# Performance work log

Measured on AMD Instinct MI355X. Metric: run time of the kernel, lower is better.

## Reference

```python
import jax, jax.numpy as jnp
import numpy as np

HID = 2048
NEXP = 16
BRD = max(64, HID // 8)        # block_router_dim = 256
BATCH, SEQ = 4, 8192
BASE_BS, MAX_BS = 512, 2048
BASE_THR, BASE_BUDGET = 0.6, 0.3


def _adjust(seq_len):
    # mirrors _adjust_parameters_for_length (static: depends only on shape)
    if seq_len <= 4096:
        return BASE_BS, BASE_THR, BASE_BUDGET
    elif seq_len <= 16384:
        return min(1024, MAX_BS), BASE_THR * 1.1, BASE_BUDGET * 0.7
    else:
        scale = min(seq_len / 16384, 4)
        return min(int(BASE_BS * scale), MAX_BS), BASE_THR * 1.2, BASE_BUDGET * (1.0 / scale)


def _layernorm(x, g, b, eps=1e-5):
    m = x.mean(-1, keepdims=True)
    v = ((x - m) ** 2).mean(-1, keepdims=True)
    return (x - m) / jnp.sqrt(v + eps) * g + b


def setup_inputs() -> dict:
    key = jax.random.key(0)
    k = jax.random.split(key, 6)
    return {
        "hidden_states": jax.random.normal(k[0], (BATCH, SEQ, HID), jnp.float32),
        # block_router: Linear(H->256) -> LN -> GELU -> Linear(256->E)
        "bw1": jax.random.normal(k[1], (HID, BRD), jnp.float32) * 0.02,
        "bb1": jnp.zeros((BRD,), jnp.float32),
        "ln_g": jnp.ones((BRD,), jnp.float32),
        "ln_b": jnp.zeros((BRD,), jnp.float32),
        # final block-router layer scaled up so block entropies spread around the
        # 0.66 threshold and both routing branches are exercised
        "bw2": jax.random.normal(k[2], (BRD, NEXP), jnp.float32) * 0.6,
        "bb2": jnp.zeros((NEXP,), jnp.float32),
        # token_router: Linear(H->H/2) -> GELU -> (Dropout: eval/identity) -> Linear(H/2->E)
        "tw1": jax.random.normal(k[3], (HID, HID // 2), jnp.float32) * 0.02,
        "tb1": jnp.zeros((HID // 2,), jnp.float32),
        "tw2": jax.random.normal(k[4], (HID // 2, NEXP), jnp.float32) * 0.02,
        "tb2": jnp.zeros((NEXP,), jnp.float32),
    }


def reference(hidden_states, bw1, bb1, ln_g, ln_b, bw2, bb2, tw1, tb1, tw2, tb2):
    B, S, H = hidden_states.shape
    E = bw2.shape[1]
    bs, thr, budget = _adjust(S)
    assert S % bs == 0, "reference assumes seq_len divisible by block_size"
    N = S // bs
    max_tok = int(S * budget)               # python int (static)
    k_budget = max(1, max_tok // bs)        # blocks_within_budget (static)

    # --- block-level routing ---
    block_repr = hidden_states.reshape(B, N, bs, H).mean(2)          # [B,N,H]
    h = _layernorm(block_repr @ bw1 + bb1, ln_g, ln_b)
    block_logits = jax.nn.gelu(h, approximate=False) @ bw2 + bb2     # [B,N,E]
    block_probs = jax.nn.softmax(block_logits, -1)
    p = block_probs + 1e-10
    entropy = -jnp.sum(p * jnp.log(p), -1) / jnp.log(jnp.float32(E))  # [B,N]

    mask1 = entropy > thr
    total_high = mask1.sum()
    # budget-based threshold adjustment (k-th largest high entropy)
    flat_ent = jnp.where(mask1.ravel(), entropy.ravel(), -jnp.inf)
    kth = jnp.sort(flat_ent)[::-1][k_budget - 1]
    cond = (total_high * bs > max_tok) & (total_high > 0) & (k_budget < total_high)
    mask2 = jnp.where(cond, entropy > kth, mask1)

    # sequential token budget over flattened (batch, block) row-major order
    cum = jnp.cumsum(mask2.ravel().astype(jnp.int32) * bs).reshape(B, N)
    token_flag = mask2 & (cum <= max_tok)            # per-token routing
    block_flag = (~mask1) | (mask2 & ~token_flag)    # block-level routing

    # block weight scatter: argmax one-hot * max prob (detached, torch uses .item())
    bw = jax.lax.stop_gradient(
        jax.nn.one_hot(jnp.argmax(block_probs, -1), E, dtype=block_probs.dtype)
        * jnp.max(block_probs, -1, keepdims=True))   # [B,N,E]

    # token-level routing computed densely, masked (dropout in eval mode = identity)
    th = jax.nn.gelu(hidden_states @ tw1 + tb1, approximate=False)
    token_probs = jax.nn.softmax(th @ tw2 + tb2, -1)  # [B,S,E]

    tf = jnp.repeat(token_flag, bs, axis=1)[..., None]   # [B,S,1]
    bf = jnp.repeat(block_flag, bs, axis=1)[..., None]
    bw_tok = jnp.repeat(bw, bs, axis=1)                  # [B,S,E]
    routing = jnp.where(tf, token_probs, jnp.where(bf, bw_tok, jnp.zeros((), hidden_states.dtype)))

    usage = routing.mean((0, 1))
    target = 1.0 / E
    aux = jnp.sum(target * jnp.log(target / (usage + 1e-10)))
    return routing, aux
```

## Files before the change

kernel.cpp:

```cpp
#include <hip/hip_runtime.h>
#include <math.h>

#define BB 4
#define SS 8192
#define HH 2048
#define EE 16
#define BRD_ 256
#define BSZ 1024
#define NN 8
#define NB 32
#define MAXTOK 1720
#define HHALF 1024
#define TC 16
#define ROWS 64
#define KSP 32
#define KL 64
#define JL 64

typedef __attribute__((ext_vector_type(8))) short bf16x8;
typedef __attribute__((ext_vector_type(4))) float f32x4;

__device__ inline short f2bf(float f) {
  unsigned u = __builtin_bit_cast(unsigned, f);
  u += 0x7FFFu + ((u >> 16) & 1u);
  return (short)(u >> 16);
}

__device__ inline void wave_flags(const double* __restrict__ ent, int l,
                                  int& flag_out, int& fb_out) {
  const double THR = 0.6 * 1.1;
  double e = (l < NB) ? ent[l] : -INFINITY;
  bool m1 = (l < NB) && (e > THR);
  unsigned long long m1mask = __ballot(m1);
  int th = __popcll(m1mask);
  double sel = m1 ? e : -INFINITY;
  #pragma unroll
  for (int o = 32; o; o >>= 1) sel = fmax(sel, __shfl_xor(sel, o));
  bool m2 = (th >= 2) ? ((l < NB) && (e > sel)) : m1;
  unsigned long long m2mask = __ballot(m2);
  int cum = __popcll(m2mask & ((2ULL << l) - 1ULL)) * BSZ;
  bool tf = m2 && (cum <= MAXTOK);
  bool bf = (l < NB) && ((!m1) || (m2 && !tf));
  flag_out = tf ? 1 : (bf ? 2 : 0);
  unsigned long long tfmask = __ballot(tf);
  fb_out = tfmask ? (__ffsll(tfmask) - 1) : -1;
}

__global__ __launch_bounds__(256) void k_bmean(const float* __restrict__ x,
                                               double* __restrict__ part) {
  int wg = blockIdx.x;
  int bn = wg >> 4, tc = wg & 15;
  int b = bn >> 3, n = bn & 7;
  int tid = threadIdx.x;
  const float* base = x + ((size_t)(b * SS + n * BSZ + tc * ROWS) * HH);
  double a0=0,a1=0,a2=0,a3=0,a4=0,a5=0,a6=0,a7=0;
  #pragma unroll 4
  for (int t = 0; t < ROWS; ++t) {
    const float4* r = (const float4*)(base + (size_t)t * HH);
    float4 u = r[tid];
    float4 v = r[tid + 256];
    a0 += u.x; a1 += u.y; a2 += u.z; a3 += u.w;
    a4 += v.x; a5 += v.y; a6 += v.z; a7 += v.w;
  }
  double* p = part + ((size_t)bn * TC + tc) * HH;
  int hA = tid * 4, hB = 1024 + tid * 4;
  p[hA] = a0; p[hA+1] = a1; p[hA+2] = a2; p[hA+3] = a3;
  p[hB] = a4; p[hB+1] = a5; p[hB+2] = a6; p[hB+3] = a7;
}

__global__ __launch_bounds__(256) void k_g1(const double* __restrict__ part,
    const float* __restrict__ bw1, double* __restrict__ g1part) {
  __shared__ double brs[NB][KL];
  __shared__ float  wsm[KL][JL];
  int bid = blockIdx.x;
  int kq = bid >> 2, jt = bid & 3;
  int k0 = kq * KL, j0 = jt * JL;
  int tid = threadIdx.x;
  #pragma unroll
  for (int i = 0; i < 8; ++i) {
    int e = i * 256 + tid;
    int bn = e >> 6, k = e & 63;
    const double* pp = part + ((size_t)bn * TC) * HH + k0 + k;
    double s = 0;
    #pragma unroll
    for (int tc = 0; tc < TC; ++tc) s += pp[(size_t)tc * HH];
    brs[bn][k] = s * (1.0 / BSZ);
  }
  #pragma unroll
  for (int i = 0; i < 4; ++i) {
    int f = i * 256 + tid;
    int r = f >> 4, c4 = f & 15;
    float4 v = *(const float4*)(bw1 + (size_t)(k0 + r) * BRD_ + j0 + c4 * 4);
    *(float4*)&wsm[r][c4 * 4] = v;
  }
  __syncthreads();
  int j = tid & 63;
  int bh = (tid >> 6) * 8;
  double acc[8];
  #pragma unroll
  for (int r = 0; r < 8; ++r) acc[r] = 0;
  #pragma unroll 8
  for (int k = 0; k < KL; ++k) {
    double wv = (double)wsm[k][j];
    #pragma unroll
    for (int r = 0; r < 8; ++r) acc[r] += brs[bh + r][k] * wv;
  }
  #pragma unroll
  for (int r = 0; r < 8; ++r)
    g1part[((size_t)kq * NB + bh + r) * BRD_ + j0 + j] = acc[r];
}

__global__ __launch_bounds__(256) void k_router2(const double* __restrict__ g1part,
    const float* __restrict__ bb1, const float* __restrict__ lng, const float* __restrict__ lnb,
    const float* __restrict__ bw2, const float* __restrict__ bb2,
    double* __restrict__ ent, float* __restrict__ bwv, int* __restrict__ bwi) {
  __shared__ double tg[BRD_];
  __shared__ double p3[16][EE];
  __shared__ double red[4];
  __shared__ double l2[EE];
  __shared__ double bcast;
  int bn = blockIdx.x, tid = threadIdx.x;

  double a = (double)bb1[tid];
  #pragma unroll
  for (int kq = 0; kq < KSP; ++kq) a += g1part[((size_t)kq * NB + bn) * BRD_ + tid];

  double v = a;
  for (int o = 32; o; o >>= 1) v += __shfl_down(v, o);
  if ((tid & 63) == 0) red[tid >> 6] = v;
  __syncthreads();
  if (tid == 0) bcast = (red[0] + red[1] + red[2] + red[3]) * (1.0 / BRD_);
  __syncthreads();
  double m = bcast;
  double d = a - m;
  v = d * d;
  for (int o = 32; o; o >>= 1) v += __shfl_down(v, o);
  if ((tid & 63) == 0) red[tid >> 6] = v;
  __syncthreads();
  if (tid == 0) bcast = (red[0] + red[1] + red[2] + red[3]) * (1.0 / BRD_);
  __syncthreads();
  double var = bcast;
  double xn = d / sqrt(var + 1e-5) * (double)lng[tid] + (double)lnb[tid];
  tg[tid] = 0.5 * xn * (1.0 + erf(xn * 0.7071067811865476));
  __syncthreads();

  {
    int e = tid & 15, jc = tid >> 4;
    double s = 0;
    const float* w2 = bw2 + (size_t)(jc * 16) * EE + e;
    #pragma unroll
    for (int jj = 0; jj < 16; ++jj) s += tg[jc * 16 + jj] * (double)w2[jj * EE];
    p3[jc][e] = s;
  }
  __syncthreads();
  if (tid < EE) {
    double acc = (double)bb2[tid];
    #pragma unroll
    for (int jc = 0; jc < 16; ++jc) acc += p3[jc][tid];
    l2[tid] = acc;
  }
  __syncthreads();

  if (tid < 64) {
    int e = tid & 15;
    double le = l2[e];
    double mx = le;
    #pragma unroll
    for (int o = 1; o < 16; o <<= 1) mx = fmax(mx, __shfl_xor(mx, o));
    double pe = exp(le - mx);
    double se = pe;
    #pragma unroll
    for (int o = 1; o < 16; o <<= 1) se += __shfl_xor(se, o);
    double pr = pe / se;
    double q = pr + 1e-10;
    double term = -q * log(q);
    double es = term;
    #pragma unroll
    for (int o = 1; o < 16; o <<= 1) es += __shfl_xor(es, o);
    double mp = pr;
    #pragma unroll
    for (int o = 1; o < 16; o <<= 1) mp = fmax(mp, __shfl_xor(mp, o));
    unsigned long long eqm = __ballot((tid < 16) && (pr == mp));
    if (tid == 0) {
      ent[bn] = es / log(16.0);
      bwv[bn] = (float)mp;
      bwi[bn] = __ffsll(eqm) - 1;
    }
  }
}

__global__ __launch_bounds__(256) void k_out(const double* __restrict__ ent,
    const float* __restrict__ bwv, const int* __restrict__ bwi,
    const float* __restrict__ x, const float* __restrict__ tw1, const float* __restrict__ tb1,
    const float* __restrict__ tw2, float* __restrict__ routing, float* __restrict__ lpart) {
  __shared__ int flg_s[NB + 1];
  __shared__ short xs_bf[64][72];
  __shared__ short wsT[64][72];
  __shared__ float ths[64][65];
  int tid = threadIdx.x;
  int bid = blockIdx.x;
  if (tid < 64) {
    int f, fb;
    wave_flags(ent, tid, f, fb);
    if (tid < NB) flg_s[tid] = f;
    if (tid == 0) flg_s[NB] = fb;
  }
  __syncthreads();

  if (bid < 256) {
    int bn = bid >> 3, seg = bid & 7;
    int fl = flg_s[bn];
    if (fl == 1) return;
    int b = bn >> 3, n = bn & 7;
    float4 z = make_float4(0.f, 0.f, 0.f, 0.f);
    float4 val = z;
    int c_hit = -1;
    if (fl == 2) {
      int ai = bwi[bn];
      c_hit = ai >> 2;
      ((float*)&val)[ai & 3] = bwv[bn];
    }
    float4* out = (float4*)(routing + ((size_t)(b * SS + n * BSZ + seg * 128) * EE));
    #pragma unroll
    for (int l = 0; l < 2; ++l) {
      int idx = l * 256 + tid;
      int c = idx & 3;
      out[idx] = (c == c_hit) ? val : z;
    }
    return;
  }

  int fb = flg_s[NB];
  if (fb < 0) return;
  int b = fb >> 3, n = fb & 7;
  int tb = bid - 256;
  int tg = tb >> 4, nc = tb & 15;
  int t0 = tg * 64, j0 = nc * 64;
  const float* xb = x + ((size_t)(b * SS + n * BSZ + t0) * HH);
  int wv = tid >> 6, lane = tid & 63;
  int wm = (wv >> 1) * 32, wn = (wv & 1) * 32;
  int fr = lane & 15, kg = lane >> 4;
  f32x4 acc00 = {0,0,0,0}, acc01 = {0,0,0,0}, acc10 = {0,0,0,0}, acc11 = {0,0,0,0};

  for (int k0 = 0; k0 < HH; k0 += 64) {
    #pragma unroll
    for (int i = 0; i < 16; ++i) {
      int e = i * 256 + tid; int r = e >> 6, c = e & 63;
      xs_bf[r][c] = f2bf(xb[(size_t)r * HH + k0 + c]);
    }
    #pragma unroll
    for (int i = 0; i < 16; ++i) {
      int e = i * 256 + tid; int r = e >> 6, c = e & 63;
      wsT[c][r] = f2bf(tw1[(size_t)(k0 + r) * HHALF + j0 + c]);
    }
    __syncthreads();
    #pragma unroll
    for (int kc = 0; kc < 64; kc += 32) {
      int ks = kc + kg * 8;
      bf16x8 a0 = *(const bf16x8*)&xs_bf[wm + fr][ks];
      bf16x8 a1 = *(const bf16x8*)&xs_bf[wm + 16 + fr][ks];
      bf16x8 b0 = *(const bf16x8*)&wsT[wn + fr][ks];
      bf16x8 b1 = *(const bf16x8*)&wsT[wn + 16 + fr][ks];
      acc00 = __builtin_amdgcn_mfma_f32_16x16x32_bf16(a0, b0, acc00, 0, 0, 0);
      acc01 = __builtin_amdgcn_mfma_f32_16x16x32_bf16(a0, b1, acc01, 0, 0, 0);
      acc10 = __builtin_amdgcn_mfma_f32_16x16x32_bf16(a1, b0, acc10, 0, 0, 0);
      acc11 = __builtin_amdgcn_mfma_f32_16x16x32_bf16(a1, b1, acc11, 0, 0, 0);
    }
    __syncthreads();
  }
  #pragma unroll
  for (int r = 0; r < 4; ++r) {
    int row0 = wm + kg * 4 + r, row1 = wm + 16 + kg * 4 + r;
    int col0 = wn + fr,         col1 = wn + 16 + fr;
    float v00 = acc00[r] + tb1[j0 + col0];
    float v01 = acc01[r] + tb1[j0 + col1];
    float v10 = acc10[r] + tb1[j0 + col0];
    float v11 = acc11[r] + tb1[j0 + col1];
    ths[row0][col0] = 0.5f * v00 * (1.0f + erff(v00 * 0.70710678f));
    ths[row0][col1] = 0.5f * v01 * (1.0f + erff(v01 * 0.70710678f));
    ths[row1][col0] = 0.5f * v10 * (1.0f + erff(v10 * 0.70710678f));
    ths[row1][col1] = 0.5f * v11 * (1.0f + erff(v11 * 0.70710678f));
  }
  __syncthreads();
  float* lp = lpart + (size_t)nc * (BSZ * EE);
  #pragma unroll
  for (int l = 0; l < 4; ++l) {
    int idx = l * 256 + tid; int t = idx >> 4, e = idx & 15;
    float s = 0;
    #pragma unroll
    for (int jj = 0; jj < 64; ++jj) s += ths[t][jj] * tw2[(size_t)(j0 + jj) * EE + e];
    lp[(t0 + t) * EE + e] = s;
  }
}

__global__ __launch_bounds__(1024) void k_tail(const double* __restrict__ ent,
    const float* __restrict__ lpart, const float* __restrict__ tb2,
    const float* __restrict__ bwv, const int* __restrict__ bwi,
    float* __restrict__ routing, float* __restrict__ outaux) {
  __shared__ int flg_s[NB + 1];
  __shared__ double up[16][EE];
  __shared__ double us[EE];
  int tid = threadIdx.x;
  if (tid < 64) {
    int f, fb;
    wave_flags(ent, tid, f, fb);
    if (tid < NB) flg_s[tid] = f;
    if (tid == 0) flg_s[NB] = fb;
  }
  __syncthreads();
  int fb = flg_s[NB];
  if (fb >= 0) {
    int b = fb >> 3, n = fb & 7;
    int t = tid;
    float l[EE];
    #pragma unroll
    for (int e = 0; e < EE; ++e) {
      float s = tb2[e];
      #pragma unroll
      for (int nc = 0; nc < 16; ++nc) s += lpart[(size_t)nc * (BSZ * EE) + t * EE + e];
      l[e] = s;
    }
    float mx = l[0];
    for (int e = 1; e < EE; ++e) mx = fmaxf(mx, l[e]);
    float se = 0;
    for (int e = 0; e < EE; ++e) { l[e] = expf(l[e] - mx); se += l[e]; }
    float inv = 1.0f / se;
    for (int e = 0; e < EE; ++e) l[e] *= inv;
    float4* orow = (float4*)(routing + ((size_t)(b * SS + n * BSZ + t) * EE));
    orow[0] = make_float4(l[0], l[1], l[2], l[3]);
    orow[1] = make_float4(l[4], l[5], l[6], l[7]);
    orow[2] = make_float4(l[8], l[9], l[10], l[11]);
    orow[3] = make_float4(l[12], l[13], l[14], l[15]);
    int w = tid >> 6;
    for (int e = 0; e < EE; ++e) {
      double v = (double)l[e];
      for (int o = 32; o; o >>= 1) v += __shfl_down(v, o);
      if ((tid & 63) == 0) up[w][e] = v;
    }
  }
  __syncthreads();
  if (tid < EE) {
    double s = 0;
    if (fb >= 0) for (int w = 0; w < 16; ++w) s += up[w][tid];
    for (int i = 0; i < NB; ++i)
      if (flg_s[i] == 2 && bwi[i] == tid) s += (double)BSZ * (double)bwv[i];
    us[tid] = s;
  }
  __syncthreads();
  if (tid == 0) {
    double aux = 0;
    const double target = 1.0 / EE;
    for (int e = 0; e < EE; ++e) {
      double u = us[e] / (double)(BB * SS);
      aux += target * log(target / (u + 1e-10));
    }
    *outaux = (float)aux;
  }
}

extern "C" void kernel_launch(void* const* d_in, const int* in_sizes, int n_in,
                              void* d_out, int out_size, void* d_ws, size_t ws_size,
                              hipStream_t stream) {
  const float* x   = (const float*)d_in[0];
  const float* bw1 = (const float*)d_in[1];
  const float* bb1 = (const float*)d_in[2];
  const float* lng = (const float*)d_in[3];
  const float* lnb = (const float*)d_in[4];
  const float* bw2 = (const float*)d_in[5];
  const float* bb2 = (const float*)d_in[6];
  const float* tw1 = (const float*)d_in[7];
  const float* tb1 = (const float*)d_in[8];
  const float* tw2 = (const float*)d_in[9];
  const float* tb2 = (const float*)d_in[10];
  float* routing = (float*)d_out;
  float* outaux = routing + (size_t)BB * SS * EE;

  char* w = (char*)d_ws;
  size_t off = 0;
  double* part  = (double*)(w + off); off += (size_t)NB * TC * HH * 8;
  double* g1p   = (double*)(w + off); off += (size_t)KSP * NB * BRD_ * 8;
  float*  lpart = (float*) (w + off); off += 16 * (size_t)BSZ * EE * 4;
  double* ent   = (double*)(w + off); off += NB * 8;
  float*  bwv   = (float*) (w + off); off += 256;
  int*    bwi   = (int*)   (w + off); off += 256;

  hipLaunchKernelGGL(k_bmean,   dim3(NB * TC), dim3(256),  0, stream, x, part);
  hipLaunchKernelGGL(k_g1,      dim3(128),     dim3(256),  0, stream, part, bw1, g1p);
  hipLaunchKernelGGL(k_router2, dim3(NB),      dim3(256),  0, stream, g1p,
                     bb1, lng, lnb, bw2, bb2, ent, bwv, bwi);
  hipLaunchKernelGGL(k_out,     dim3(512),     dim3(256),  0, stream, ent, bwv, bwi,
                     x, tw1, tb1, tw2, routing, lpart);
  hipLaunchKernelGGL(k_tail,    dim3(1),       dim3(1024), 0, stream, ent, lpart, tb2,
                     bwv, bwi, routing, outaux);
}
```

Baseline: 75.12 us.

## Fuse five kernels into two using last-block-done atomic counters

```diff
diff --git a/kernel.cpp b/kernel.cpp
--- a/kernel.cpp
+++ b/kernel.cpp
@@ -11,11 +11,8 @@
 #define NB 32
 #define MAXTOK 1720
 #define HHALF 1024
-#define TC 16
-#define ROWS 64
-#define KSP 32
-#define KL 64
-#define JL 64
+#define TC 32
+#define ROWS 32
 
 typedef __attribute__((ext_vector_type(8))) short bf16x8;
 typedef __attribute__((ext_vector_type(4))) float f32x4;
@@ -46,84 +43,79 @@
   fb_out = tfmask ? (__ffsll(tfmask) - 1) : -1;
 }
 
-__global__ __launch_bounds__(256) void k_bmean(const float* __restrict__ x,
-                                               double* __restrict__ part) {
-  int wg = blockIdx.x;
-  int bn = wg >> 4, tc = wg & 15;
-  int b = bn >> 3, n = bn & 7;
-  int tid = threadIdx.x;
-  const float* base = x + ((size_t)(b * SS + n * BSZ + tc * ROWS) * HH);
-  double a0=0,a1=0,a2=0,a3=0,a4=0,a5=0,a6=0,a7=0;
-  #pragma unroll 4
-  for (int t = 0; t < ROWS; ++t) {
-    const float4* r = (const float4*)(base + (size_t)t * HH);
-    float4 u = r[tid];
-    float4 v = r[tid + 256];
-    a0 += u.x; a1 += u.y; a2 += u.z; a3 += u.w;
-    a4 += v.x; a5 += v.y; a6 += v.z; a7 += v.w;
-  }
-  double* p = part + ((size_t)bn * TC + tc) * HH;
-  int hA = tid * 4, hB = 1024 + tid * 4;
-  p[hA] = a0; p[hA+1] = a1; p[hA+2] = a2; p[hA+3] = a3;
-  p[hB] = a4; p[hB+1] = a5; p[hB+2] = a6; p[hB+3] = a7;
-}
-
-__global__ __launch_bounds__(256) void k_g1(const double* __restrict__ part,
-    const float* __restrict__ bw1, double* __restrict__ g1part) {
-  __shared__ double brs[NB][KL];
-  __shared__ float  wsm[KL][JL];
-  int bid = blockIdx.x;
-  int kq = bid >> 2, jt = bid & 3;
-  int k0 = kq * KL, j0 = jt * JL;
-  int tid = threadIdx.x;
-  #pragma unroll
-  for (int i = 0; i < 8; ++i) {
-    int e = i * 256 + tid;
-    int bn = e >> 6, k = e & 63;
-    const double* pp = part + ((size_t)bn * TC) * HH + k0 + k;
-    double s = 0;
-    #pragma unroll
-    for (int tc = 0; tc < TC; ++tc) s += pp[(size_t)tc * HH];
-    brs[bn][k] = s * (1.0 / BSZ);
-  }
-  #pragma unroll
-  for (int i = 0; i < 4; ++i) {
-    int f = i * 256 + tid;
-    int r = f >> 4, c4 = f & 15;
-    float4 v = *(const float4*)(bw1 + (size_t)(k0 + r) * BRD_ + j0 + c4 * 4);
-    *(float4*)&wsm[r][c4 * 4] = v;
-  }
-  __syncthreads();
-  int j = tid & 63;
-  int bh = (tid >> 6) * 8;
-  double acc[8];
-  #pragma unroll
-  for (int r = 0; r < 8; ++r) acc[r] = 0;
-  #pragma unroll 8
-  for (int k = 0; k < KL; ++k) {
-    double wv = (double)wsm[k][j];
-    #pragma unroll
-    for (int r = 0; r < 8; ++r) acc[r] += brs[bh + r][k] * wv;
-  }
-  #pragma unroll
-  for (int r = 0; r < 8; ++r)
-    g1part[((size_t)kq * NB + bh + r) * BRD_ + j0 + j] = acc[r];
-}
-
-__global__ __launch_bounds__(256) void k_router2(const double* __restrict__ g1part,
-    const float* __restrict__ bb1, const float* __restrict__ lng, const float* __restrict__ lnb,
+__global__ __launch_bounds__(256, 4) void k_main(const float* __restrict__ x,
+    double* __restrict__ part,
+    const float* __restrict__ bw1, const float* __restrict__ bb1,
+    const float* __restrict__ lng, const float* __restrict__ lnb,
     const float* __restrict__ bw2, const float* __restrict__ bb2,
-    double* __restrict__ ent, float* __restrict__ bwv, int* __restrict__ bwi) {
+    double* __restrict__ ent, float* __restrict__ bwv, int* __restrict__ bwi,
+    int* __restrict__ cnt) {
+  __shared__ double brs[HH];
+  __shared__ double p2[4][BRD_];
   __shared__ double tg[BRD_];
   __shared__ double p3[16][EE];
   __shared__ double red[4];
   __shared__ double l2[EE];
   __shared__ double bcast;
-  int bn = blockIdx.x, tid = threadIdx.x;
-
-  double a = (double)bb1[tid];
+  __shared__ int lastf;
+  int wg = blockIdx.x, tid = threadIdx.x;
+  int bn = wg >> 5, tc = wg & 31;
+  int b = bn >> 3, n = bn & 7;
+
+  const float* base = x + ((size_t)(b * SS + n * BSZ + tc * ROWS) * HH);
+  {
+    double a0=0,a1=0,a2=0,a3=0,a4=0,a5=0,a6=0,a7=0;
+    #pragma unroll 4
+    for (int t = 0; t < ROWS; ++t) {
+      const float4* r = (const float4*)(base + (size_t)t * HH);
+      float4 u = r[tid];
+      float4 v = r[tid + 256];
+      a0 += u.x; a1 += u.y; a2 += u.z; a3 += u.w;
+      a4 += v.x; a5 += v.y; a6 += v.z; a7 += v.w;
+    }
+    double* p = part + ((size_t)bn * TC + tc) * HH;
+    int hA = tid * 4, hB = 1024 + tid * 4;
+    p[hA] = a0; p[hA+1] = a1; p[hA+2] = a2; p[hA+3] = a3;
+    p[hB] = a4; p[hB+1] = a5; p[hB+2] = a6; p[hB+3] = a7;
+  }
+  __syncthreads();
+  if (tid == 0) {
+    int r = __hip_atomic_fetch_add(cnt + bn, 1, __ATOMIC_ACQ_REL,
+                                   __HIP_MEMORY_SCOPE_AGENT);
+    lastf = (r == TC - 1);
+  }
+  __syncthreads();
+  if (!lastf) return;
+
   #pragma unroll
-  for (int kq = 0; kq < KSP; ++kq) a += g1part[((size_t)kq * NB + bn) * BRD_ + tid];
+  for (int i = 0; i < 8; ++i) {
+    int h = i * 256 + tid;
+    const double* pp = part + ((size_t)bn * TC) * HH + h;
+    double s = 0;
+    #pragma unroll
+    for (int t = 0; t < TC; ++t) s += pp[(size_t)t * HH];
+    brs[h] = s * (1.0 / BSZ);
+  }
+  __syncthreads();
+
+  {
+    int j0 = (tid & 63) * 4, kq = tid >> 6;
+    const float* wp = bw1 + (size_t)(kq * 512) * BRD_ + j0;
+    const double* brk = brs + kq * 512;
+    double a0=0,a1=0,a2=0,a3=0,c0=0,c1=0,c2=0,c3=0;
+    #pragma unroll 8
+    for (int k = 0; k < 512; k += 2) {
+      float4 w0 = *(const float4*)(wp + (size_t)k * BRD_);
+      float4 w1 = *(const float4*)(wp + (size_t)(k + 1) * BRD_);
+      double bk0 = brk[k], bk1 = brk[k + 1];
+      a0 += bk0 * w0.x; a1 += bk0 * w0.y; a2 += bk0 * w0.z; a3 += bk0 * w0.w;
+      c0 += bk1 * w1.x; c1 += bk1 * w1.y; c2 += bk1 * w1.z; c3 += bk1 * w1.w;
+    }
+    p2[kq][j0]   = a0 + c0; p2[kq][j0+1] = a1 + c1;
+    p2[kq][j0+2] = a2 + c2; p2[kq][j0+3] = a3 + c3;
+  }
+  __syncthreads();
+  double a = (double)bb1[tid] + p2[0][tid] + p2[1][tid] + p2[2][tid] + p2[3][tid];
 
   double v = a;
   for (int o = 32; o; o >>= 1) v += __shfl_down(v, o);
@@ -189,14 +181,19 @@
   }
 }
 
-__global__ __launch_bounds__(256) void k_out(const double* __restrict__ ent,
+__global__ __launch_bounds__(256) void k_out2(const double* __restrict__ ent,
     const float* __restrict__ bwv, const int* __restrict__ bwi,
     const float* __restrict__ x, const float* __restrict__ tw1, const float* __restrict__ tb1,
-    const float* __restrict__ tw2, float* __restrict__ routing, float* __restrict__ lpart) {
+    const float* __restrict__ tw2, const float* __restrict__ tb2,
+    float* __restrict__ routing, float* __restrict__ lpart,
+    float* __restrict__ outaux, int* __restrict__ cnt2) {
   __shared__ int flg_s[NB + 1];
   __shared__ short xs_bf[64][72];
   __shared__ short wsT[64][72];
   __shared__ float ths[64][65];
+  __shared__ double up[4][EE];
+  __shared__ double us[EE];
+  __shared__ int lastf;
   int tid = threadIdx.x;
   int bid = blockIdx.x;
   if (tid < 64) {
@@ -206,142 +203,140 @@
     if (tid == 0) flg_s[NB] = fb;
   }
   __syncthreads();
+  int fb = flg_s[NB];
 
   if (bid < 256) {
     int bn = bid >> 3, seg = bid & 7;
     int fl = flg_s[bn];
-    if (fl == 1) return;
-    int b = bn >> 3, n = bn & 7;
-    float4 z = make_float4(0.f, 0.f, 0.f, 0.f);
-    float4 val = z;
-    int c_hit = -1;
-    if (fl == 2) {
-      int ai = bwi[bn];
-      c_hit = ai >> 2;
-      ((float*)&val)[ai & 3] = bwv[bn];
-    }
-    float4* out = (float4*)(routing + ((size_t)(b * SS + n * BSZ + seg * 128) * EE));
-    #pragma unroll
-    for (int l = 0; l < 2; ++l) {
-      int idx = l * 256 + tid;
-      int c = idx & 3;
-      out[idx] = (c == c_hit) ? val : z;
-    }
-    return;
-  }
-
-  int fb = flg_s[NB];
-  if (fb < 0) return;
-  int b = fb >> 3, n = fb & 7;
-  int tb = bid - 256;
-  int tg = tb >> 4, nc = tb & 15;
-  int t0 = tg * 64, j0 = nc * 64;
-  const float* xb = x + ((size_t)(b * SS + n * BSZ + t0) * HH);
-  int wv = tid >> 6, lane = tid & 63;
-  int wm = (wv >> 1) * 32, wn = (wv & 1) * 32;
-  int fr = lane & 15, kg = lane >> 4;
-  f32x4 acc00 = {0,0,0,0}, acc01 = {0,0,0,0}, acc10 = {0,0,0,0}, acc11 = {0,0,0,0};
-
-  for (int k0 = 0; k0 < HH; k0 += 64) {
-    #pragma unroll
-    for (int i = 0; i < 16; ++i) {
-      int e = i * 256 + tid; int r = e >> 6, c = e & 63;
-      xs_bf[r][c] = f2bf(xb[(size_t)r * HH + k0 + c]);
-    }
-    #pragma unroll
-    for (int i = 0; i < 16; ++i) {
-      int e = i * 256 + tid; int r = e >> 6, c = e & 63;
-      wsT[c][r] = f2bf(tw1[(size_t)(k0 + r) * HHALF + j0 + c]);
+    if (fl != 1) {
+      int b = bn >> 3, n = bn & 7;
+      float4 z = make_float4(0.f, 0.f, 0.f, 0.f);
+      float4 val = z;
+      int c_hit = -1;
+      if (fl == 2) {
+        int ai = bwi[bn];
+        c_hit = ai >> 2;
+        ((float*)&val)[ai & 3] = bwv[bn];
+      }
+      float4* out = (float4*)(routing + ((size_t)(b * SS + n * BSZ + seg * 128) * EE));
+      #pragma unroll
+      for (int l = 0; l < 2; ++l) {
+        int idx = l * 256 + tid;
+        int c = idx & 3;
+        out[idx] = (c == c_hit) ? val : z;
+      }
+    }
+  } else if (fb >= 0) {
+    int b = fb >> 3, n = fb & 7;
+    int tb = bid - 256;
+    int tg = tb >> 4, nc = tb & 15;
+    int t0 = tg * 64, j0 = nc * 64;
+    const float* xb = x + ((size_t)(b * SS + n * BSZ + t0) * HH);
+    int wv = tid >> 6, lane = tid & 63;
+    int wm = (wv >> 1) * 32, wn = (wv & 1) * 32;
+    int fr = lane & 15, kg = lane >> 4;
+    f32x4 acc00 = {0,0,0,0}, acc01 = {0,0,0,0}, acc10 = {0,0,0,0}, acc11 = {0,0,0,0};
+    for (int k0 = 0; k0 < HH; k0 += 64) {
+      #pragma unroll
+      for (int i = 0; i < 16; ++i) {
+        int e = i * 256 + tid; int r = e >> 6, c = e & 63;
+        xs_bf[r][c] = f2bf(xb[(size_t)r * HH + k0 + c]);
+      }
+      #pragma unroll
+      for (int i = 0; i < 16; ++i) {
+        int e = i * 256 + tid; int r = e >> 6, c = e & 63;
+        wsT[c][r] = f2bf(tw1[(size_t)(k0 + r) * HHALF + j0 + c]);
+      }
+      __syncthreads();
+      #pragma unroll
+      for (int kc = 0; kc < 64; kc += 32) {
+        int ks = kc + kg * 8;
+        bf16x8 a0 = *(const bf16x8*)&xs_bf[wm + fr][ks];
+        bf16x8 a1 = *(const bf16x8*)&xs_bf[wm + 16 + fr][ks];
+        bf16x8 b0 = *(const bf16x8*)&wsT[wn + fr][ks];
+        bf16x8 b1 = *(const bf16x8*)&wsT[wn + 16 + fr][ks];
+        acc00 = __builtin_amdgcn_mfma_f32_16x16x32_bf16(a0, b0, acc00, 0, 0, 0);
+        acc01 = __builtin_amdgcn_mfma_f32_16x16x32_bf16(a0, b1, acc01, 0, 0, 0);
+        acc10 = __builtin_amdgcn_mfma_f32_16x16x32_bf16(a1, b0, acc10, 0, 0, 0);
+        acc11 = __builtin_amdgcn_mfma_f32_16x16x32_bf16(a1, b1, acc11, 0, 0, 0);
+      }
+      __syncthreads();
+    }
+    #pragma unroll
+    for (int r = 0; r < 4; ++r) {
+      int row0 = wm + kg * 4 + r, row1 = wm + 16 + kg * 4 + r;
+      int col0 = wn + fr,         col1 = wn + 16 + fr;
+      float v00 = acc00[r] + tb1[j0 + col0];
+      float v01 = acc01[r] + tb1[j0 + col1];
+      float v10 = acc10[r] + tb1[j0 + col0];
+      float v11 = acc11[r] + tb1[j0 + col1];
+      ths[row0][col0] = 0.5f * v00 * (1.0f + erff(v00 * 0.70710678f));
+      ths[row0][col1] = 0.5f * v01 * (1.0f + erff(v01 * 0.70710678f));
+      ths[row1][col0] = 0.5f * v10 * (1.0f + erff(v10 * 0.70710678f));
+      ths[row1][col1] = 0.5f * v11 * (1.0f + erff(v11 * 0.70710678f));
     }
     __syncthreads();
-    #pragma unroll
-    for (int kc = 0; kc < 64; kc += 32) {
-      int ks = kc + kg * 8;
-      bf16x8 a0 = *(const bf16x8*)&xs_bf[wm + fr][ks];
-      bf16x8 a1 = *(const bf16x8*)&xs_bf[wm + 16 + fr][ks];
-      bf16x8 b0 = *(const bf16x8*)&wsT[wn + fr][ks];
-      bf16x8 b1 = *(const bf16x8*)&wsT[wn + 16 + fr][ks];
-      acc00 = __builtin_amdgcn_mfma_f32_16x16x32_bf16(a0, b0, acc00, 0, 0, 0);
-      acc01 = __builtin_amdgcn_mfma_f32_16x16x32_bf16(a0, b1, acc01, 0, 0, 0);
-      acc10 = __builtin_amdgcn_mfma_f32_16x16x32_bf16(a1, b0, acc10, 0, 0, 0);
-      acc11 = __builtin_amdgcn_mfma_f32_16x16x32_bf16(a1, b1, acc11, 0, 0, 0);
-    }
-    __syncthreads();
-  }
+    float* lp = lpart + (size_t)nc * (BSZ * EE);
+    #pragma unroll
+    for (int l = 0; l < 4; ++l) {
+      int idx = l * 256 + tid; int t = idx >> 4, e = idx & 15;
+      float s = 0;
+      #pragma unroll
+      for (int jj = 0; jj < 64; ++jj) s += ths[t][jj] * tw2[(size_t)(j0 + jj) * EE + e];
+      lp[(t0 + t) * EE + e] = s;
+    }
+  }
+
+  __syncthreads();
+  if (tid == 0) {
+    int r = __hip_atomic_fetch_add(cnt2, 1, __ATOMIC_ACQ_REL,
+                                   __HIP_MEMORY_SCOPE_AGENT);
+    lastf = (r == 511);
+  }
+  __syncthreads();
+  if (!lastf) return;
+
+  double us_p[EE];
   #pragma unroll
-  for (int r = 0; r < 4; ++r) {
-    int row0 = wm + kg * 4 + r, row1 = wm + 16 + kg * 4 + r;
-    int col0 = wn + fr,         col1 = wn + 16 + fr;
-    float v00 = acc00[r] + tb1[j0 + col0];
-    float v01 = acc01[r] + tb1[j0 + col1];
-    float v10 = acc10[r] + tb1[j0 + col0];
-    float v11 = acc11[r] + tb1[j0 + col1];
-    ths[row0][col0] = 0.5f * v00 * (1.0f + erff(v00 * 0.70710678f));
-    ths[row0][col1] = 0.5f * v01 * (1.0f + erff(v01 * 0.70710678f));
-    ths[row1][col0] = 0.5f * v10 * (1.0f + erff(v10 * 0.70710678f));
-    ths[row1][col1] = 0.5f * v11 * (1.0f + erff(v11 * 0.70710678f));
-  }
-  __syncthreads();
-  float* lp = lpart + (size_t)nc * (BSZ * EE);
-  #pragma unroll
-  for (int l = 0; l < 4; ++l) {
-    int idx = l * 256 + tid; int t = idx >> 4, e = idx & 15;
-    float s = 0;
-    #pragma unroll
-    for (int jj = 0; jj < 64; ++jj) s += ths[t][jj] * tw2[(size_t)(j0 + jj) * EE + e];
-    lp[(t0 + t) * EE + e] = s;
-  }
-}
-
-__global__ __launch_bounds__(1024) void k_tail(const double* __restrict__ ent,
-    const float* __restrict__ lpart, const float* __restrict__ tb2,
-    const float* __restrict__ bwv, const int* __restrict__ bwi,
-    float* __restrict__ routing, float* __restrict__ outaux) {
-  __shared__ int flg_s[NB + 1];
-  __shared__ double up[16][EE];
-  __shared__ double us[EE];
-  int tid = threadIdx.x;
-  if (tid < 64) {
-    int f, fb;
-    wave_flags(ent, tid, f, fb);
-    if (tid < NB) flg_s[tid] = f;
-    if (tid == 0) flg_s[NB] = fb;
-  }
-  __syncthreads();
-  int fb = flg_s[NB];
+  for (int e = 0; e < EE; ++e) us_p[e] = 0;
   if (fb >= 0) {
     int b = fb >> 3, n = fb & 7;
-    int t = tid;
-    float l[EE];
-    #pragma unroll
-    for (int e = 0; e < EE; ++e) {
-      float s = tb2[e];
-      #pragma unroll
-      for (int nc = 0; nc < 16; ++nc) s += lpart[(size_t)nc * (BSZ * EE) + t * EE + e];
-      l[e] = s;
-    }
-    float mx = l[0];
-    for (int e = 1; e < EE; ++e) mx = fmaxf(mx, l[e]);
-    float se = 0;
-    for (int e = 0; e < EE; ++e) { l[e] = expf(l[e] - mx); se += l[e]; }
-    float inv = 1.0f / se;
-    for (int e = 0; e < EE; ++e) l[e] *= inv;
-    float4* orow = (float4*)(routing + ((size_t)(b * SS + n * BSZ + t) * EE));
-    orow[0] = make_float4(l[0], l[1], l[2], l[3]);
-    orow[1] = make_float4(l[4], l[5], l[6], l[7]);
-    orow[2] = make_float4(l[8], l[9], l[10], l[11]);
-    orow[3] = make_float4(l[12], l[13], l[14], l[15]);
-    int w = tid >> 6;
-    for (int e = 0; e < EE; ++e) {
-      double v = (double)l[e];
-      for (int o = 32; o; o >>= 1) v += __shfl_down(v, o);
-      if ((tid & 63) == 0) up[w][e] = v;
-    }
+    for (int rep = 0; rep < 4; ++rep) {
+      int t = rep * 256 + tid;
+      float l[EE];
+      #pragma unroll
+      for (int e = 0; e < EE; ++e) {
+        float s = tb2[e];
+        #pragma unroll
+        for (int nc = 0; nc < 16; ++nc) s += lpart[(size_t)nc * (BSZ * EE) + t * EE + e];
+        l[e] = s;
+      }
+      float mx = l[0];
+      for (int e = 1; e < EE; ++e) mx = fmaxf(mx, l[e]);
+      float se = 0;
+      for (int e = 0; e < EE; ++e) { l[e] = expf(l[e] - mx); se += l[e]; }
+      float inv = 1.0f / se;
+      for (int e = 0; e < EE; ++e) l[e] *= inv;
+      float4* orow = (float4*)(routing + ((size_t)(b * SS + n * BSZ + t) * EE));
+      orow[0] = make_float4(l[0], l[1], l[2], l[3]);
+      orow[1] = make_float4(l[4], l[5], l[6], l[7]);
+      orow[2] = make_float4(l[8], l[9], l[10], l[11]);
+      orow[3] = make_float4(l[12], l[13], l[14], l[15]);
+      #pragma unroll
+      for (int e = 0; e < EE; ++e) us_p[e] += (double)l[e];
+    }
+  }
+  int w = tid >> 6;
+  #pragma unroll
+  for (int e = 0; e < EE; ++e) {
+    double v = us_p[e];
+    for (int o = 32; o; o >>= 1) v += __shfl_down(v, o);
+    if ((tid & 63) == 0) up[w][e] = v;
   }
   __syncthreads();
   if (tid < EE) {
     double s = 0;
-    if (fb >= 0) for (int w = 0; w < 16; ++w) s += up[w][tid];
+    if (fb >= 0) for (int ww = 0; ww < 4; ++ww) s += up[ww][tid];
     for (int i = 0; i < NB; ++i)
       if (flg_s[i] == 2 && bwi[i] == tid) s += (double)BSZ * (double)bwv[i];
     us[tid] = s;
@@ -378,18 +373,15 @@
   char* w = (char*)d_ws;
   size_t off = 0;
   double* part  = (double*)(w + off); off += (size_t)NB * TC * HH * 8;
-  double* g1p   = (double*)(w + off); off += (size_t)KSP * NB * BRD_ * 8;
   float*  lpart = (float*) (w + off); off += 16 * (size_t)BSZ * EE * 4;
   double* ent   = (double*)(w + off); off += NB * 8;
   float*  bwv   = (float*) (w + off); off += 256;
   int*    bwi   = (int*)   (w + off); off += 256;
-
-  hipLaunchKernelGGL(k_bmean,   dim3(NB * TC), dim3(256),  0, stream, x, part);
-  hipLaunchKernelGGL(k_g1,      dim3(128),     dim3(256),  0, stream, part, bw1, g1p);
-  hipLaunchKernelGGL(k_router2, dim3(NB),      dim3(256),  0, stream, g1p,
-                     bb1, lng, lnb, bw2, bb2, ent, bwv, bwi);
-  hipLaunchKernelGGL(k_out,     dim3(512),     dim3(256),  0, stream, ent, bwv, bwi,
-                     x, tw1, tb1, tw2, routing, lpart);
-  hipLaunchKernelGGL(k_tail,    dim3(1),       dim3(1024), 0, stream, ent, lpart, tb2,
-                     bwv, bwi, routing, outaux);
-}
+  int*    cnt   = (int*)   (w + off); off += 256;
+
+  hipMemsetAsync(cnt, 0, 256, stream);
+  hipLaunchKernelGGL(k_main, dim3(NB * TC), dim3(256), 0, stream, x, part,
+                     bw1, bb1, lng, lnb, bw2, bb2, ent, bwv, bwi, cnt);
+  hipLaunchKernelGGL(k_out2, dim3(512),     dim3(256), 0, stream, ent, bwv, bwi,
+                     x, tw1, tb1, tw2, tb2, routing, lpart, outaux, cnt + NB);
+}
```

New measurement: 221.1 us. 194% more time.
